# Kernel optimization log

Hardware: AMD Instinct MI355X
Metric: run time of the kernel (lower is better)

The kernel has to match this reference:

```python
import jax, jax.numpy as jnp
import numpy as np

N, C, SD, A, H = 1048576, 8192, 32, 4, 64


def _xavier(key, shape):
    fan_in, fan_out = shape
    lim = np.sqrt(6.0 / (fan_in + fan_out)).astype(np.float32)
    return jax.random.uniform(key, shape, jnp.float32, -lim, lim)


def setup_inputs() -> dict:
    key = jax.random.key(0)
    ks = jax.random.split(key, 10)
    return {
        "cell_state": jax.random.normal(ks[0], (N, SD), jnp.float32),
        "arch_state": jax.random.uniform(ks[1], (N, A), jnp.float32),
        "energy": jax.random.uniform(ks[2], (N,), jnp.float32),
        "phi_local": jax.random.uniform(ks[3], (N,), jnp.float32),
        "W1": _xavier(ks[4], (SD + A, H)),
        "b1": jnp.zeros((H,), jnp.float32),
        "W2": _xavier(ks[5], (H, 1)),
        "b2": jnp.zeros((1,), jnp.float32),
        "Wc1": _xavier(ks[6], (A + 3, H // 2)),
        "bc1": jnp.zeros((H // 2,), jnp.float32),
        "Wc2": _xavier(ks[7], (H // 2, 1)),
        "bc2": jnp.zeros((1,), jnp.float32),
        "segment_ids": jnp.sort(jax.random.randint(ks[8], (N,), 0, C, jnp.int32)),
        "n_clusters": C,
    }


def reference(cell_state, arch_state, energy, phi_local,
              W1, b1, W2, b2, Wc1, bc1, Wc2, bc2,
              segment_ids, n_clusters):
    seg = segment_ids
    nc = n_clusters
    seg_sum = lambda v: jax.ops.segment_sum(v, seg, num_segments=nc)

    # ---- cells -> clusters ----
    x = jnp.concatenate([cell_state, arch_state], axis=-1)          # [N, SD+A]
    h = jax.nn.relu(x @ W1 + b1)                                    # [N, H]
    base = jax.nn.sigmoid(h @ W2 + b2)[:, 0]                        # [N]
    importance = jnp.clip(base * energy * phi_local, 0.01, 1.0)
    w = importance * energy * phi_local                              # cell weight

    counts = seg_sum(jnp.ones_like(w))                               # [C]
    wsum = seg_sum(w)                                                # [C]
    safe_cnt = jnp.maximum(counts, 1.0)
    # normalized weights; uniform fallback when a cluster's weight sum is 0
    norm_w = jnp.where(wsum[seg] > 0,
                       w / jnp.maximum(wsum, 1e-30)[seg],
                       1.0 / safe_cnt[seg])
    aggregate = seg_sum(norm_w[:, None] * arch_state)                # [C, A]

    # unbiased per-dim variance averaged over dims (torch .var(dim=0).mean())
    mean = seg_sum(arch_state) / safe_cnt[:, None]                   # [C, A]
    sqdev = seg_sum((arch_state - mean[seg]) ** 2)                   # [C, A]
    var = jnp.where(counts >= 2.0,
                    sqdev.mean(-1) / jnp.maximum(counts - 1.0, 1.0),
                    0.0)                                             # [C]
    phi_cluster = 1.0 - jnp.minimum(1.0, var * 2.0)
    coherence = 1.0 - var

    # ---- clusters -> organism ----
    feats = jnp.concatenate([aggregate,
                             phi_cluster[:, None],
                             coherence[:, None],
                             jnp.minimum(1.0, counts / 20.0)[:, None]], axis=-1)  # [C, A+3]
    hc = jax.nn.relu(feats @ Wc1 + bc1)
    basec = jax.nn.sigmoid(hc @ Wc2 + bc2)[:, 0]                     # [C]
    impc = jnp.clip(basec * phi_cluster, 0.01, 1.0)
    valid = counts > 0
    wc = jnp.where(valid, impc * counts, 0.0)
    wc_sum = wc.sum()
    nvalid = jnp.maximum(valid.sum().astype(jnp.float32), 1.0)
    norm_wc = jnp.where(wc_sum > 0,
                        wc / jnp.maximum(wc_sum, 1e-30),
                        valid.astype(jnp.float32) / nvalid)
    global_archetype = (norm_wc[:, None] * aggregate).sum(0)         # [A]

    return aggregate, phi_cluster, coherence, global_archetype
```

## Files before the change

kernel.cpp:

```cpp
#include <hip/hip_runtime.h>
#include <hip/hip_bf16.h>

#define NC 8192
#define SDIM 32
#define ADIM 4
#define XDIM 36
#define HDIM 64
#define MLP_BLOCKS 1024

typedef _Float16 half8 __attribute__((ext_vector_type(8)));
typedef _Float16 half4 __attribute__((ext_vector_type(4)));
typedef float f32x4 __attribute__((ext_vector_type(4)));

__device__ __forceinline__ float sigmoidf_(float t) {
    return 1.0f / (1.0f + __expf(-t));
}

__global__ __launch_bounds__(256) void bounds_kernel(
    const int* __restrict__ seg, int* __restrict__ startx,
    int* __restrict__ endx, int n)
{
    const int i = blockIdx.x * 256 + threadIdx.x;
    if (i >= n) return;
    const int s = seg[i];
    if (i == 0) {
        startx[s] = 0;
        for (int c = 0; c < s; ++c) { startx[c] = 0; endx[c] = 0; }
    } else {
        const int sp = seg[i - 1];
        if (sp != s) {
            startx[s] = i;
            for (int c = sp + 1; c < s; ++c) { startx[c] = i; endx[c] = i; }
        }
    }
    if (i == n - 1) {
        endx[s] = n;
        for (int c = s + 1; c < NC; ++c) { startx[c] = n; endx[c] = n; }
    } else if (seg[i + 1] != s) {
        endx[s] = i + 1;
    }
}

__global__ __launch_bounds__(256, 4) void mlp_kernel(
    const float* __restrict__ cell_state,
    const float* __restrict__ arch_state,
    const float* __restrict__ energy,
    const float* __restrict__ phi_local,
    const float* __restrict__ W1,
    const float* __restrict__ b1,
    const float* __restrict__ W2,
    const float* __restrict__ b2,
    float* __restrict__ w_out,
    int n)
{
    __shared__ _Float16 xs[256 * 40];
    __shared__ half8 wpack[8 * 64];
    const int tid  = threadIdx.x;
    const int lane = tid & 63;
    const int l15  = lane & 15;
    const int lg   = lane >> 4;
    const int wv   = tid >> 6;

    #pragma unroll
    for (int fo = 0; fo < 2; ++fo) {
        const int f  = 2 * wv + fo;
        const int nt = f >> 1;
        const int s  = f & 1;
        half8 v = {};
        #pragma unroll
        for (int jj = 0; jj < 8; ++jj) {
            const int k = 32 * s + lg * 8 + jj;
            float wvv = 0.0f;
            if (k < XDIM)       wvv = W1[k * HDIM + 16 * nt + l15];
            else if (k == XDIM) wvv = b1[16 * nt + l15];
            v[jj] = (_Float16)wvv;
        }
        wpack[f * 64 + lane] = v;
    }
    __syncthreads();

    half8 af[4][2];
    #pragma unroll
    for (int nt = 0; nt < 4; ++nt)
        #pragma unroll
        for (int s = 0; s < 2; ++s)
            af[nt][s] = wpack[(nt * 2 + s) * 64 + lane];

    float w2v[16];
    #pragma unroll
    for (int nt = 0; nt < 4; ++nt)
        #pragma unroll
        for (int q = 0; q < 4; ++q)
            w2v[nt * 4 + q] = W2[16 * nt + lg * 4 + q];
    const float sb2 = b2[0];

    const float4* cell4 = reinterpret_cast<const float4*>(cell_state);
    const float4* arch4 = reinterpret_cast<const float4*>(arch_state);

    #pragma unroll 1
    for (int cb = blockIdx.x * 256; cb < n; cb += gridDim.x * 256) {
        __syncthreads();

        #pragma unroll
        for (int uu = 0; uu < 8; ++uu) {
            const int u   = uu * 256 + tid;
            const int row = u >> 3;
            const int c4  = u & 7;
            float4 v = {0.f, 0.f, 0.f, 0.f};
            if (cb + row < n) v = cell4[(size_t)cb * 8 + u];
            half4 h;
            h[0] = (_Float16)v.x; h[1] = (_Float16)v.y;
            h[2] = (_Float16)v.z; h[3] = (_Float16)v.w;
            *reinterpret_cast<half4*>(&xs[row * 40 + c4 * 4]) = h;
        }
        {
            const int row = tid;
            float4 a = {0.f, 0.f, 0.f, 0.f};
            if (cb + row < n) a = arch4[cb + row];
            half4 h;
            h[0] = (_Float16)a.x; h[1] = (_Float16)a.y;
            h[2] = (_Float16)a.z; h[3] = (_Float16)a.w;
            *reinterpret_cast<half4*>(&xs[row * 40 + 32]) = h;
            half4 hb;
            hb[0] = (_Float16)1.0f; hb[1] = (_Float16)0.0f;
            hb[2] = (_Float16)0.0f; hb[3] = (_Float16)0.0f;
            *reinterpret_cast<half4*>(&xs[row * 40 + 36]) = hb;
        }
        __syncthreads();

        float acc = 0.0f;
        #pragma unroll
        for (int t = 0; t < 4; ++t) {
            const int r = wv * 64 + 16 * t + l15;
            const half8 x0 = *reinterpret_cast<const half8*>(&xs[r * 40 + lg * 8]);
            half8 x1 = {};
            if (lg == 0)
                x1 = *reinterpret_cast<const half8*>(&xs[r * 40 + 32]);

            float pq = 0.0f;
            #pragma unroll
            for (int nt = 0; nt < 4; ++nt) {
                f32x4 cc = f32x4{0.f, 0.f, 0.f, 0.f};
                cc = __builtin_amdgcn_mfma_f32_16x16x32_f16(af[nt][0], x0, cc, 0, 0, 0);
                cc = __builtin_amdgcn_mfma_f32_16x16x32_f16(af[nt][1], x1, cc, 0, 0, 0);
                #pragma unroll
                for (int q = 0; q < 4; ++q)
                    pq = __builtin_fmaf(fmaxf(cc[q], 0.0f), w2v[nt * 4 + q], pq);
            }
            pq += __shfl_xor(pq, 16);
            pq += __shfl_xor(pq, 32);
            if (lg == t) acc = pq;
        }
        const float base = sigmoidf_(acc + sb2);

        const int gid = cb + wv * 64 + lane;
        if (gid < n) {
            const float ep = energy[gid] * phi_local[gid];
            const float imp = fminf(fmaxf(base * ep, 0.01f), 1.0f);
            w_out[gid] = imp * ep;
        }
    }
}

__global__ __launch_bounds__(256) void cluster_kernel(
    const float* __restrict__ arch_state,
    const float* __restrict__ w_arr,
    const int*   __restrict__ startx,
    const int*   __restrict__ endx,
    const float* __restrict__ Wc1,
    const float* __restrict__ bc1,
    const float* __restrict__ Wc2,
    const float* __restrict__ bc2,
    float* __restrict__ out,
    float* __restrict__ ws2)
{
    const int lane = threadIdx.x & 63;
    const int c = blockIdx.x * 4 + (threadIdx.x >> 6);
    const int s0 = startx[c];
    const int e0 = endx[c];

    float pw = 0.0f;
    float pa0 = 0.f, pa1 = 0.f, pa2 = 0.f, pa3 = 0.f;
    float pw0 = 0.f, pw1 = 0.f, pw2 = 0.f, pw3 = 0.f;
    float pq0 = 0.f, pq1 = 0.f, pq2 = 0.f, pq3 = 0.f;
    const float4* arch4 = reinterpret_cast<const float4*>(arch_state);

    int i = s0 + lane;
    bool vcur = i < e0;
    float4 ac = {}; float wcur = 0.0f;
    if (vcur) { ac = arch4[i]; wcur = w_arr[i]; }
    while (vcur) {
        const int j = i + 64;
        const bool vnext = j < e0;
        float4 an = {}; float wnext = 0.0f;
        if (vnext) { an = arch4[j]; wnext = w_arr[j]; }
        pw += wcur;
        pa0 += ac.x; pa1 += ac.y; pa2 += ac.z; pa3 += ac.w;
        pw0 = __builtin_fmaf(wcur, ac.x, pw0); pw1 = __builtin_fmaf(wcur, ac.y, pw1);
        pw2 = __builtin_fmaf(wcur, ac.z, pw2); pw3 = __builtin_fmaf(wcur, ac.w, pw3);
        pq0 = __builtin_fmaf(ac.x, ac.x, pq0); pq1 = __builtin_fmaf(ac.y, ac.y, pq1);
        pq2 = __builtin_fmaf(ac.z, ac.z, pq2); pq3 = __builtin_fmaf(ac.w, ac.w, pq3);
        i = j; vcur = vnext; ac = an; wcur = wnext;
    }
#define RED13(F) F(pw) F(pa0) F(pa1) F(pa2) F(pa3) \
                 F(pw0) F(pw1) F(pw2) F(pw3) F(pq0) F(pq1) F(pq2) F(pq3)
#define BFLY(V) V += __shfl_xor(V, off_);
    #pragma unroll
    for (int off_ = 1; off_ < 64; off_ <<= 1) { RED13(BFLY) }

    const float cnt = (float)(e0 - s0);
    const float safe_cnt = fmaxf(cnt, 1.0f);
    const float wsum = pw;

    float agg[4];
    if (wsum > 0.0f) {
        const float inv = 1.0f / fmaxf(wsum, 1e-30f);
        agg[0] = pw0 * inv; agg[1] = pw1 * inv;
        agg[2] = pw2 * inv; agg[3] = pw3 * inv;
    } else {
        const float inv = 1.0f / safe_cnt;
        agg[0] = pa0 * inv; agg[1] = pa1 * inv;
        agg[2] = pa2 * inv; agg[3] = pa3 * inv;
    }

    const float sA[4]  = { pa0, pa1, pa2, pa3 };
    const float sA2[4] = { pq0, pq1, pq2, pq3 };
    float sq = 0.0f;
    #pragma unroll
    for (int d = 0; d < 4; ++d) {
        const float mean = sA[d] / safe_cnt;
        const float s2 = sA2[d] - 2.0f * mean * sA[d] + cnt * mean * mean;
        sq += fmaxf(s2, 0.0f);
    }
    const float var = (cnt >= 2.0f) ? (sq * 0.25f) / fmaxf(cnt - 1.0f, 1.0f) : 0.0f;
    const float phi_c = 1.0f - fminf(1.0f, var * 2.0f);
    const float coh = 1.0f - var;

    const float feats[7] = { agg[0], agg[1], agg[2], agg[3],
                             phi_c, coh, fminf(1.0f, cnt * 0.05f) };
    float t = bc2[0];
    #pragma unroll
    for (int j = 0; j < 32; ++j) {
        float hj = bc1[j];
        #pragma unroll
        for (int k = 0; k < 7; ++k)
            hj = __builtin_fmaf(feats[k], Wc1[k * 32 + j], hj);
        t += fmaxf(hj, 0.0f) * Wc2[j];
    }
    const float basec = sigmoidf_(t);
    const float impc = fminf(fmaxf(basec * phi_c, 0.01f), 1.0f);
    const bool valid = cnt > 0.0f;
    const float wc = valid ? impc * cnt : 0.0f;
    const float vf = valid ? 1.0f : 0.0f;

    if (lane == 0) {
        out[c * 4 + 0] = agg[0]; out[c * 4 + 1] = agg[1];
        out[c * 4 + 2] = agg[2]; out[c * 4 + 3] = agg[3];
        out[NC * 4 + c] = phi_c;
        out[NC * 5 + c] = coh;
        ws2[0 * NC + c] = wc;
        ws2[1 * NC + c] = vf;
        #pragma unroll
        for (int d = 0; d < 4; ++d) ws2[(2 + d) * NC + c] = wc * agg[d];
        #pragma unroll
        for (int d = 0; d < 4; ++d) ws2[(6 + d) * NC + c] = vf * agg[d];
    }
}

__global__ __launch_bounds__(1024) void finalize_kernel(
    const float* __restrict__ ws2, float* __restrict__ out)
{
    __shared__ float red[16][10];
    const int tid = threadIdx.x;
    const int lane = tid & 63;
    const int wv = tid >> 6;

    float r[10];
    #pragma unroll
    for (int k = 0; k < 10; ++k) r[k] = 0.0f;
    for (int c = tid; c < NC; c += 1024) {
        #pragma unroll
        for (int k = 0; k < 10; ++k) r[k] += ws2[k * NC + c];
    }
    #pragma unroll
    for (int off = 1; off < 64; off <<= 1) {
        #pragma unroll
        for (int k = 0; k < 10; ++k) r[k] += __shfl_xor(r[k], off);
    }
    if (lane == 0) {
        #pragma unroll
        for (int k = 0; k < 10; ++k) red[wv][k] = r[k];
    }
    __syncthreads();
    if (tid == 0) {
        float g[10];
        #pragma unroll
        for (int k = 0; k < 10; ++k) {
            float acc = 0.0f;
            for (int i = 0; i < 16; ++i) acc += red[i][k];
            g[k] = acc;
        }
        const float wcs = g[0];
        const float nv = fmaxf(g[1], 1.0f);
        #pragma unroll
        for (int d = 0; d < 4; ++d) {
            out[NC * 6 + d] = (wcs > 0.0f) ? g[2 + d] / fmaxf(wcs, 1e-30f)
                                           : g[6 + d] / nv;
        }
    }
}

extern "C" void kernel_launch(void* const* d_in, const int* in_sizes, int n_in,
                              void* d_out, int out_size, void* d_ws, size_t ws_size,
                              hipStream_t stream) {
    const float* cell_state = (const float*)d_in[0];
    const float* arch_state = (const float*)d_in[1];
    const float* energy     = (const float*)d_in[2];
    const float* phi_local  = (const float*)d_in[3];
    const float* W1  = (const float*)d_in[4];
    const float* b1  = (const float*)d_in[5];
    const float* W2  = (const float*)d_in[6];
    const float* b2  = (const float*)d_in[7];
    const float* Wc1 = (const float*)d_in[8];
    const float* bc1 = (const float*)d_in[9];
    const float* Wc2 = (const float*)d_in[10];
    const float* bc2 = (const float*)d_in[11];
    const int* seg   = (const int*)d_in[12];

    const int n = in_sizes[2];
    float* out = (float*)d_out;

    float* w_arr = (float*)d_ws;
    int* startx  = (int*)(w_arr + n);
    int* endx    = startx + NC;
    float* ws2   = (float*)(endx + NC);

    bounds_kernel<<<(n + 255) / 256, 256, 0, stream>>>(seg, startx, endx, n);
    mlp_kernel<<<MLP_BLOCKS, 256, 0, stream>>>(cell_state, arch_state, energy,
                                               phi_local, W1, b1, W2, b2,
                                               w_arr, n);
    cluster_kernel<<<NC / 4, 256, 0, stream>>>(arch_state, w_arr, startx, endx,
                                               Wc1, bc1, Wc2, bc2, out, ws2);
    finalize_kernel<<<1, 1024, 0, stream>>>(ws2, out);
}
```

Measured before the change: 64.58 us.

## Software-pipeline MLP kernel global loads into registers for next tile

Register-prefetches the next tile's cell_state and arch_state rows while the current tile's MFMA work runs, replacing the load-then-convert pattern inside each iteration. The syncthreads pair becomes explicit s_barrier calls with an lgkmcnt wait and a sched_barrier to keep load issue ahead of compute. Out-of-range rows are clamped to the last row instead of zero-filled. This hides global memory latency behind compute at the cost of more VGPRs (nine float4 values held across the loop), which may reduce occupancy.

```diff
diff --git a/kernel.cpp b/kernel.cpp
--- a/kernel.cpp
+++ b/kernel.cpp
@@ -96,37 +96,56 @@
 
     const float4* cell4 = reinterpret_cast<const float4*>(cell_state);
     const float4* arch4 = reinterpret_cast<const float4*>(arch_state);
+    const int stride = gridDim.x * 256;
+
+    float4 pc[8]; float4 pa;
+
+#define ISSUE_STAGE_LOADS(CB)                                                 \
+    {                                                                         \
+        _Pragma("unroll")                                                     \
+        for (int uu = 0; uu < 8; ++uu) {                                      \
+            const int u = uu * 256 + tid;                                     \
+            int row = (CB) + (u >> 3);                                        \
+            if (row >= n) row = n - 1;                                        \
+            pc[uu] = cell4[(size_t)row * 8 + (u & 7)];                        \
+        }                                                                     \
+        int arow = (CB) + tid; if (arow >= n) arow = n - 1;                   \
+        pa = arch4[arow];                                                     \
+    }
+
+    int cb = blockIdx.x * 256;
+    ISSUE_STAGE_LOADS(cb);
 
     #pragma unroll 1
-    for (int cb = blockIdx.x * 256; cb < n; cb += gridDim.x * 256) {
-        __syncthreads();
-
+    while (cb < n) {
         #pragma unroll
         for (int uu = 0; uu < 8; ++uu) {
             const int u   = uu * 256 + tid;
             const int row = u >> 3;
             const int c4  = u & 7;
-            float4 v = {0.f, 0.f, 0.f, 0.f};
-            if (cb + row < n) v = cell4[(size_t)cb * 8 + u];
             half4 h;
-            h[0] = (_Float16)v.x; h[1] = (_Float16)v.y;
-            h[2] = (_Float16)v.z; h[3] = (_Float16)v.w;
+            h[0] = (_Float16)pc[uu].x; h[1] = (_Float16)pc[uu].y;
+            h[2] = (_Float16)pc[uu].z; h[3] = (_Float16)pc[uu].w;
             *reinterpret_cast<half4*>(&xs[row * 40 + c4 * 4]) = h;
         }
         {
-            const int row = tid;
-            float4 a = {0.f, 0.f, 0.f, 0.f};
-            if (cb + row < n) a = arch4[cb + row];
             half4 h;
-            h[0] = (_Float16)a.x; h[1] = (_Float16)a.y;
-            h[2] = (_Float16)a.z; h[3] = (_Float16)a.w;
-            *reinterpret_cast<half4*>(&xs[row * 40 + 32]) = h;
+            h[0] = (_Float16)pa.x; h[1] = (_Float16)pa.y;
+            h[2] = (_Float16)pa.z; h[3] = (_Float16)pa.w;
+            *reinterpret_cast<half4*>(&xs[tid * 40 + 32]) = h;
             half4 hb;
             hb[0] = (_Float16)1.0f; hb[1] = (_Float16)0.0f;
             hb[2] = (_Float16)0.0f; hb[3] = (_Float16)0.0f;
-            *reinterpret_cast<half4*>(&xs[row * 40 + 36]) = hb;
-        }
-        __syncthreads();
+            *reinterpret_cast<half4*>(&xs[tid * 40 + 36]) = hb;
+        }
+
+        const int cur = cb;
+        cb += stride;
+        if (cb < n) ISSUE_STAGE_LOADS(cb);
+        __builtin_amdgcn_sched_barrier(0);
+
+        asm volatile("s_waitcnt lgkmcnt(0)" ::: "memory");
+        __builtin_amdgcn_s_barrier();
 
         float acc = 0.0f;
         #pragma unroll
@@ -153,13 +172,16 @@
         }
         const float base = sigmoidf_(acc + sb2);
 
-        const int gid = cb + wv * 64 + lane;
+        const int gid = cur + wv * 64 + lane;
         if (gid < n) {
             const float ep = energy[gid] * phi_local[gid];
             const float imp = fminf(fmaxf(base * ep, 0.01f), 1.0f);
             w_out[gid] = imp * ep;
         }
-    }
+
+        __builtin_amdgcn_s_barrier();
+    }
+#undef ISSUE_STAGE_LOADS
 }
 
 __global__ __launch_bounds__(256) void cluster_kernel(
```

Result: slower. 66.67 us (+3.2%).
